# Optimization experiments

Hardware: AMD Instinct MI355X
Metric: run time of the kernel (lower is better)

## Reference

```python
import jax, jax.numpy as jnp
import numpy as np

INF = 1.0e9
B, NI, NJ = 1, 768, 768
C_NODE, C_PAIR = 512, 128
H, C_HID = 8, 32
LN_EPS = 1e-5


def _ln(x, w, b):
    m = jnp.mean(x, axis=-1, keepdims=True)
    v = jnp.mean(jnp.square(x - m), axis=-1, keepdims=True)
    return (x - m) * jax.lax.rsqrt(v + LN_EPS) * w + b


def setup_inputs() -> dict:
    key = jax.random.key(0)
    ks = jax.random.split(key, 16)
    s_node = 1.0 / np.sqrt(C_NODE)
    s_pair = 1.0 / np.sqrt(C_PAIR)
    s_hid = 1.0 / np.sqrt(H * C_HID)
    inp = {
        "node_embed_i": jax.random.normal(ks[0], (B, NI, C_NODE), jnp.float32),
        "node_embed_j": jax.random.normal(ks[1], (B, NJ, C_NODE), jnp.float32),
        "pair_embed": jax.random.normal(ks[2], (B, NI, NJ, C_PAIR), jnp.float32),
        "pair_mask": (jax.random.uniform(ks[3], (B, NI, NJ)) < 0.95).astype(jnp.float32),
        "node_mask_i": (jax.random.uniform(ks[4], (B, NI)) < 0.98).astype(jnp.float32),
        # LayerNorm params
        "ln_i_w": jnp.ones((C_NODE,), jnp.float32), "ln_i_b": jnp.zeros((C_NODE,), jnp.float32),
        "ln_j_w": jnp.ones((C_NODE,), jnp.float32), "ln_j_b": jnp.zeros((C_NODE,), jnp.float32),
        "ln_p_w": jnp.ones((C_PAIR,), jnp.float32), "ln_p_b": jnp.zeros((C_PAIR,), jnp.float32),
        # pair-bias projection and its gate: Linear(C_PAIR, H)
        "W_pb": jax.random.normal(ks[5], (C_PAIR, H), jnp.float32) * s_pair,
        "b_pb": jnp.zeros((H,), jnp.float32),
        "W_pg": jax.random.normal(ks[6], (C_PAIR, H), jnp.float32) * s_pair,
        "b_pg": jnp.zeros((H,), jnp.float32),
        # attention projections (q/k/v bias-free, OpenFold-style)
        "Wq": jax.random.normal(ks[7], (C_NODE, H * C_HID), jnp.float32) * s_node,
        "Wk": jax.random.normal(ks[8], (C_NODE, H * C_HID), jnp.float32) * s_node,
        "Wv": jax.random.normal(ks[9], (C_NODE, H * C_HID), jnp.float32) * s_node,
        # output gate and output projection
        "Wg": jax.random.normal(ks[10], (C_NODE, H * C_HID), jnp.float32) * s_node,
        "bg": jnp.zeros((H * C_HID,), jnp.float32),
        "Wo": jax.random.normal(ks[11], (H * C_HID, C_NODE), jnp.float32) * s_hid,
        "bo": jnp.zeros((C_NODE,), jnp.float32),
    }
    return inp


def reference(node_embed_i, node_embed_j, pair_embed, pair_mask, node_mask_i,
              ln_i_w, ln_i_b, ln_j_w, ln_j_b, ln_p_w, ln_p_b,
              W_pb, b_pb, W_pg, b_pg, Wq, Wk, Wv, Wg, bg, Wo, bo):
    # LayerNorms
    qx = _ln(node_embed_i, ln_i_w, ln_i_b)           # [B,NI,C_NODE]
    kx = _ln(node_embed_j, ln_j_w, ln_j_b)           # [B,NJ,C_NODE]
    p = _ln(pair_embed, ln_p_w, ln_p_b)              # [B,NI,NJ,C_PAIR]

    # additive mask bias: 0 where valid, -inf where masked; broadcast over heads
    mask_bias = (INF * (pair_mask - 1.0))[:, None, :, :]          # [B,1,NI,NJ]

    # gated pair bias -> [B,H,NI,NJ] (permute_final_dims([2,0,1]))
    pb = (p @ W_pb + b_pb) * jax.nn.sigmoid(p @ W_pg + b_pg)      # [B,NI,NJ,H]
    pair_bias = jnp.transpose(pb, (0, 3, 1, 2))

    # multi-head attention with injected biases
    q = (qx @ Wq).reshape(B, NI, H, C_HID) * (C_HID ** -0.5)
    k = (kx @ Wk).reshape(B, NJ, H, C_HID)
    v = (kx @ Wv).reshape(B, NJ, H, C_HID)
    scores = jnp.einsum('bihc,bjhc->bhij', q, k) + mask_bias + pair_bias
    a = jax.nn.softmax(scores, axis=-1)                           # [B,H,NI,NJ]
    o = jnp.einsum('bhij,bjhc->bihc', a, v)                       # [B,NI,H,C_HID]

    # sigmoid output gate, flatten heads, output projection
    g = jax.nn.sigmoid(qx @ Wg + bg).reshape(B, NI, H, C_HID)
    o = (o * g).reshape(B, NI, H * C_HID)
    mha_out = o @ Wo + bo                                         # [B,NI,C_NODE]

    # residual on the layernormed input, scaled by node mask (dropout = identity at inference)
    return qx + mha_out * node_mask_i[..., None]
```

## Files before the change

### kernel.cpp

```cpp
#include <hip/hip_runtime.h>
#include <hip/hip_bf16.h>

#define NI 768
#define NJ 768
#define CN 512
#define CP 128
#define NH 8
#define CH 32
#define HC 256

typedef float  fx4  __attribute__((ext_vector_type(4)));
typedef float  fx2  __attribute__((ext_vector_type(2)));
typedef short  bv8  __attribute__((ext_vector_type(8)));

__device__ __forceinline__ short f2bf(float f) {
    __hip_bfloat16 h = __float2bfloat16(f);
    return *reinterpret_cast<short*>(&h);
}
__device__ __forceinline__ float bf2f(unsigned short u) {
    union { unsigned int u; float f; } c; c.u = ((unsigned int)u) << 16; return c.f;
}

__global__ __launch_bounds__(256) void fused_front_kernel(
    const float* __restrict__ node_i, const float* __restrict__ node_j,
    const float* __restrict__ ln_i_w, const float* __restrict__ ln_i_b,
    const float* __restrict__ ln_j_w, const float* __restrict__ ln_j_b,
    const float* __restrict__ Wq, const float* __restrict__ Wk,
    const float* __restrict__ Wv, const float* __restrict__ Wg,
    const float* __restrict__ bg,
    const float* __restrict__ lnpw, const float* __restrict__ lnpb,
    const float* __restrict__ Wpb, const float* __restrict__ bpb,
    const float* __restrict__ Wpg, const float* __restrict__ bpg,
    const float* __restrict__ pair, const float* __restrict__ pmask,
    float* __restrict__ qx, unsigned short* __restrict__ qsb,
    unsigned short* __restrict__ ksb, unsigned short* __restrict__ vtb,
    float* __restrict__ gs, float* __restrict__ bias)
{
    const int bid = blockIdx.x;
    const int t = threadIdx.x;
    if (bid < 192) {
        __shared__ float xs[8][CN];
        __shared__ float red[4][8][2];
        const bool isj = bid >= 96;
        const int r0 = (isj ? bid - 96 : bid) * 8;
        const float* xin = isj ? node_j : node_i;
        const float* lw = isj ? ln_j_w : ln_i_w;
        const float* lb = isj ? ln_j_b : ln_i_b;
        const int wv = t >> 6;

        fx2 vrow[8]; float s8[8], q8[8];
#pragma unroll
        for (int r = 0; r < 8; ++r) {
            vrow[r] = *(const fx2*)(xin + (size_t)(r0 + r) * CN + t * 2);
            s8[r] = vrow[r][0] + vrow[r][1];
            q8[r] = vrow[r][0] * vrow[r][0] + vrow[r][1] * vrow[r][1];
        }
#pragma unroll
        for (int d = 1; d < 64; d <<= 1)
#pragma unroll
            for (int r = 0; r < 8; ++r) {
                s8[r] += __shfl_xor(s8[r], d);
                q8[r] += __shfl_xor(q8[r], d);
            }
        if ((t & 63) == 0)
#pragma unroll
            for (int r = 0; r < 8; ++r) { red[wv][r][0] = s8[r]; red[wv][r][1] = q8[r]; }
        __syncthreads();
        fx2 lwv = *(const fx2*)(lw + t * 2), lbv = *(const fx2*)(lb + t * 2);
#pragma unroll
        for (int r = 0; r < 8; ++r) {
            float s = red[0][r][0] + red[1][r][0] + red[2][r][0] + red[3][r][0];
            float q = red[0][r][1] + red[1][r][1] + red[2][r][1] + red[3][r][1];
            float mean = s * (1.f / CN);
            float var = q * (1.f / CN) - mean * mean;
            float rs = rsqrtf(var + 1e-5f);
            fx2 o;
            o[0] = (vrow[r][0] - mean) * rs * lwv[0] + lbv[0];
            o[1] = (vrow[r][1] - mean) * rs * lwv[1] + lbv[1];
            xs[r][t * 2] = o[0]; xs[r][t * 2 + 1] = o[1];
            if (!isj) *(fx2*)(qx + (size_t)(r0 + r) * CN + t * 2) = o;
        }
        __syncthreads();

        for (int m = 0; m < 2; ++m) {
            const float* W = isj ? (m ? Wv : Wk) : (m ? Wg : Wq);
            float acc[8] = {0.f,0.f,0.f,0.f,0.f,0.f,0.f,0.f};
            for (int cc = 0; cc < CN; cc += 4) {
                fx4 xv[8];
#pragma unroll
                for (int r = 0; r < 8; ++r) xv[r] = *(const fx4*)&xs[r][cc];
#pragma unroll
                for (int u = 0; u < 4; ++u) {
                    float w = W[(size_t)(cc + u) * HC + t];
#pragma unroll
                    for (int r = 0; r < 8; ++r) acc[r] = fmaf(xv[r][u], w, acc[r]);
                }
            }
            if (!isj) {
                if (m == 0) {
#pragma unroll
                    for (int r = 0; r < 8; ++r)
                        qsb[(size_t)(r0 + r) * HC + t] =
                            (unsigned short)f2bf(acc[r] * 0.17677669529663687f);
                } else {
#pragma unroll
                    for (int r = 0; r < 8; ++r)
                        gs[(size_t)(r0 + r) * HC + t] =
                            1.f / (1.f + __expf(-(acc[r] + bg[t])));
                }
            } else {
                if (m == 0) {
#pragma unroll
                    for (int r = 0; r < 8; ++r)
                        ksb[(size_t)(r0 + r) * HC + t] = (unsigned short)f2bf(acc[r]);
                } else {
                    bv8 vv;
#pragma unroll
                    for (int r = 0; r < 8; ++r) vv[r] = f2bf(acc[r]);
                    *(bv8*)&vtb[(size_t)t * NJ + r0] = vv;
                }
            }
        }
        return;
    }

    __shared__ unsigned short wcatT[16][136];
    __shared__ float redS[16][16], redC[16][16];
    __shared__ float scalS[16], scalC[16];
    {
        const int o = t & 15, cg = t >> 4;
        float pS = 0.f, pC = 0.f;
#pragma unroll
        for (int e = 0; e < 8; ++e) {
            int c = cg * 8 + e;
            float w = (o < 8) ? Wpb[c * 8 + o] : Wpg[c * 8 + (o - 8)];
            float wv = lnpw[c] * w;
            short b = f2bf(wv);
            wcatT[o][c] = (unsigned short)b;
            pS += bf2f((unsigned short)b);
            pC += lnpb[c] * w;
        }
        redS[cg][o] = pS; redC[cg][o] = pC;
        __syncthreads();
        if (t < 16) {
            float s = 0.f, c2 = 0.f;
#pragma unroll
            for (int k = 0; k < 16; ++k) { s += redS[k][t]; c2 += redC[k][t]; }
            scalS[t] = s;
            scalC[t] = c2 + ((t < 8) ? bpb[t] : bpg[t - 8]);
        }
        __syncthreads();
    }

    const int lane = t & 63;
    const int wave = t >> 6;
    const int tile = (bid - 192) * 4 + wave;
    const int i  = tile / (NJ / 16);
    const int jt = (tile % (NJ / 16)) * 16;
    const int o  = lane & 15;
    const int kq = lane >> 4;

    bv8 bfrag[4];
#pragma unroll
    for (int s = 0; s < 4; ++s)
        bfrag[s] = *(const bv8*)&wcatT[o][s * 32 + kq * 8];

    const float spb = scalS[o];
    const float cpb = scalC[o];

    const float* prow = pair + ((size_t)i * NJ + (jt + o)) * CP + kq * 8;
    fx4 x0[4], x1[4];
#pragma unroll
    for (int s = 0; s < 4; ++s) {
        x0[s] = *(const fx4*)(prow + s * 32);
        x1[s] = *(const fx4*)(prow + s * 32 + 4);
    }
    float sum = 0.f, ssq = 0.f;
    bv8 afrag[4];
#pragma unroll
    for (int s = 0; s < 4; ++s) {
#pragma unroll
        for (int u = 0; u < 4; ++u) {
            float a = x0[s][u], b = x1[s][u];
            sum += a + b;
            ssq = fmaf(a, a, ssq);
            ssq = fmaf(b, b, ssq);
            afrag[s][u]     = f2bf(a);
            afrag[s][u + 4] = f2bf(b);
        }
    }
    sum += __shfl_xor(sum, 16); ssq += __shfl_xor(ssq, 16);
    sum += __shfl_xor(sum, 32); ssq += __shfl_xor(ssq, 32);

    fx4 acc = {0.f, 0.f, 0.f, 0.f};
#pragma unroll
    for (int s = 0; s < 4; ++s)
        acc = __builtin_amdgcn_mfma_f32_16x16x32_bf16(afrag[s], bfrag[s], acc, 0, 0, 0);

#pragma unroll
    for (int r = 0; r < 4; ++r) {
        const int p = kq * 4 + r;
        float sp = __shfl(sum, p);
        float qp = __shfl(ssq, p);
        float mean = sp * (1.f / CP);
        float var  = qp * (1.f / CP) - mean * mean;
        float rstd = rsqrtf(var + 1e-5f);
        float pre  = rstd * (acc[r] - mean * spb) + cpb;
        float part = __shfl_xor(pre, 8);
        if (o < 8) {
            float sig = 1.f / (1.f + __expf(-part));
            int j = jt + p;
            float b = pre * sig + (pmask[(size_t)i * NJ + j] - 1.f) * 1.0e9f;
            bias[((size_t)o * NI + i) * NJ + j] = b;
        }
    }
}

__global__ __launch_bounds__(256) void attn_kernel(
    const short* __restrict__ qsb, const short* __restrict__ ksb,
    const short* __restrict__ vtb, const float* __restrict__ bias,
    float* __restrict__ pnum, float* __restrict__ pden)
{
    __shared__ unsigned short P[32][392];
    __shared__ float sumbuf[4][32];
    const int i0 = blockIdx.x * 32;
    const int h  = blockIdx.y;
    const int jh = blockIdx.z;
    const int jbase = jh * 384;
    const int pb = ((int)blockIdx.x * NH + h) * 2 + jh;
    const int t = threadIdx.x;
    const int w = t >> 6;
    const int lane = t & 63;
    const int rowl = lane & 15;
    const int g = lane >> 4;

    bv8 aq[2];
#pragma unroll
    for (int it = 0; it < 2; ++it)
        aq[it] = *(const bv8*)&qsb[(size_t)(i0 + it * 16 + rowl) * HC + h * CH + g * 8];

    float rs[2][4] = {{0.f,0.f,0.f,0.f},{0.f,0.f,0.f,0.f}};
    for (int jt = 0; jt < 6; ++jt) {
        const int jloc = w * 96 + jt * 16;
        const int jb = jbase + jloc;
        bv8 bk = *(const bv8*)&ksb[(size_t)(jb + rowl) * HC + h * CH + g * 8];
#pragma unroll
        for (int it = 0; it < 2; ++it) {
            fx4 acc = {0.f, 0.f, 0.f, 0.f};
            acc = __builtin_amdgcn_mfma_f32_16x16x32_bf16(aq[it], bk, acc, 0, 0, 0);
#pragma unroll
            for (int r = 0; r < 4; ++r) {
                const int il = it * 16 + g * 4 + r;
                float s = acc[r] + bias[((size_t)h * NI + (i0 + il)) * NJ + jb + rowl];
                float p = __expf(s);
                rs[it][r] += p;
                P[il][jloc + rowl] = (unsigned short)f2bf(p);
            }
        }
    }
#pragma unroll
    for (int it = 0; it < 2; ++it)
#pragma unroll
        for (int r = 0; r < 4; ++r) {
            float v = rs[it][r];
            v += __shfl_xor(v, 1); v += __shfl_xor(v, 2);
            v += __shfl_xor(v, 4); v += __shfl_xor(v, 8);
            rs[it][r] = v;
        }
    if (rowl == 0) {
#pragma unroll
        for (int it = 0; it < 2; ++it)
#pragma unroll
            for (int r = 0; r < 4; ++r)
                sumbuf[w][it * 16 + g * 4 + r] = rs[it][r];
    }
    __syncthreads();

    if (t < 32)
        pden[(size_t)pb * 32 + t] =
            sumbuf[0][t] + sumbuf[1][t] + sumbuf[2][t] + sumbuf[3][t];

    const int it = w & 1, ct = w >> 1;
    fx4 acc = {0.f, 0.f, 0.f, 0.f};
    for (int kk = 0; kk < 12; ++kk) {
        const int jloc = kk * 32;
        bv8 ap = *(const bv8*)&P[it * 16 + rowl][jloc + g * 8];
        bv8 bv = *(const bv8*)&vtb[(size_t)(h * CH + ct * 16 + rowl) * NJ + jbase + jloc + g * 8];
        acc = __builtin_amdgcn_mfma_f32_16x16x32_bf16(ap, bv, acc, 0, 0, 0);
    }
#pragma unroll
    for (int r = 0; r < 4; ++r) {
        const int il = it * 16 + g * 4 + r;
        pnum[(size_t)pb * 1024 + il * 32 + ct * 16 + rowl] = acc[r];
    }
}

__global__ __launch_bounds__(256) void combine_out_kernel(
    const float* __restrict__ pnum, const float* __restrict__ pden,
    const float* __restrict__ gs, const float* __restrict__ qx,
    const float* __restrict__ Wo, const float* __restrict__ bo,
    const float* __restrict__ mi, float* __restrict__ outp)
{
    __shared__ float ogl[2][HC];
    const int r0 = blockIdx.x * 2;
    const int t = threadIdx.x;
    const int h = t >> 5, c = t & 31;
#pragma unroll
    for (int r = 0; r < 2; ++r) {
        const int i = r0 + r;
        const int pb = ((i >> 5) * NH + h) * 2;
        const int il = i & 31;
        float n = pnum[(size_t)(pb + 0) * 1024 + il * 32 + c]
                + pnum[(size_t)(pb + 1) * 1024 + il * 32 + c];
        float d = pden[(size_t)(pb + 0) * 32 + il]
                + pden[(size_t)(pb + 1) * 32 + il];
        ogl[r][t] = n / d * gs[(size_t)i * HC + t];
    }
    __syncthreads();

    float acc[2][2] = {{0,0},{0,0}};
    for (int cc = 0; cc < HC; cc += 4) {
        fx4 xr0 = *(const fx4*)&ogl[0][cc];
        fx4 xr1 = *(const fx4*)&ogl[1][cc];
#pragma unroll
        for (int u = 0; u < 4; ++u) {
            float w0 = Wo[(size_t)(cc + u) * CN + t];
            float w1 = Wo[(size_t)(cc + u) * CN + 256 + t];
            acc[0][0] = fmaf(xr0[u], w0, acc[0][0]); acc[0][1] = fmaf(xr0[u], w1, acc[0][1]);
            acc[1][0] = fmaf(xr1[u], w0, acc[1][0]); acc[1][1] = fmaf(xr1[u], w1, acc[1][1]);
        }
    }
#pragma unroll
    for (int r = 0; r < 2; ++r) {
        float mk = mi[r0 + r];
        size_t base = (size_t)(r0 + r) * CN;
        outp[base + t]       = qx[base + t]       + (acc[r][0] + bo[t])       * mk;
        outp[base + 256 + t] = qx[base + 256 + t] + (acc[r][1] + bo[t + 256]) * mk;
    }
}

extern "C" void kernel_launch(void* const* d_in, const int* in_sizes, int n_in,
                              void* d_out, int out_size, void* d_ws, size_t ws_size,
                              hipStream_t stream)
{
    const float* node_i = (const float*)d_in[0];
    const float* node_j = (const float*)d_in[1];
    const float* pair   = (const float*)d_in[2];
    const float* pmask  = (const float*)d_in[3];
    const float* nmask  = (const float*)d_in[4];
    const float* ln_i_w = (const float*)d_in[5];
    const float* ln_i_b = (const float*)d_in[6];
    const float* ln_j_w = (const float*)d_in[7];
    const float* ln_j_b = (const float*)d_in[8];
    const float* ln_p_w = (const float*)d_in[9];
    const float* ln_p_b = (const float*)d_in[10];
    const float* W_pb   = (const float*)d_in[11];
    const float* b_pb   = (const float*)d_in[12];
    const float* W_pg   = (const float*)d_in[13];
    const float* b_pg   = (const float*)d_in[14];
    const float* Wq     = (const float*)d_in[15];
    const float* Wk     = (const float*)d_in[16];
    const float* Wv     = (const float*)d_in[17];
    const float* Wg     = (const float*)d_in[18];
    const float* bg     = (const float*)d_in[19];
    const float* Wo     = (const float*)d_in[20];
    const float* bo     = (const float*)d_in[21];
    float* outp = (float*)d_out;

    float* fw = (float*)d_ws;
    float* qx   = fw;
    float* gs   = qx + (size_t)NI * CN;
    float* bias = gs + (size_t)NI * HC;
    float* pnum = bias + (size_t)NH * NI * NJ;
    float* pden = pnum + (size_t)24 * NH * 2 * 1024;
    unsigned short* qsb = (unsigned short*)(pden + (size_t)24 * NH * 2 * 32);
    unsigned short* ksb = qsb + (size_t)NI * HC;
    unsigned short* vtb = ksb + (size_t)NJ * HC;

    hipLaunchKernelGGL(fused_front_kernel, dim3(192 + (NI * NJ) / 64), dim3(256), 0, stream,
                       node_i, node_j, ln_i_w, ln_i_b, ln_j_w, ln_j_b,
                       Wq, Wk, Wv, Wg, bg,
                       ln_p_w, ln_p_b, W_pb, b_pb, W_pg, b_pg,
                       pair, pmask,
                       qx, qsb, ksb, vtb, gs, bias);
    hipLaunchKernelGGL(attn_kernel, dim3(NI / 32, NH, 2), dim3(256), 0, stream,
                       (const short*)qsb, (const short*)ksb, (const short*)vtb,
                       bias, pnum, pden);
    hipLaunchKernelGGL(combine_out_kernel, dim3(NI / 2), dim3(256), 0, stream,
                       pnum, pden, gs, qx, Wo, bo, nmask, outp);
}
```

Baseline: 112.0 us.

## Store pair bias as bf16 via LDS-staged writes and drop split-J attention partials

The pair-bias tensor (8×768×768) is now written as bf16 instead of fp32. Each front block covers 64 contiguous j positions and stages results in shared memory so it can emit vectorized row stores instead of scattered 4-byte writes. The attention kernel no longer splits J in two. Each block handles the full 768 columns with a larger P buffer and normalizes and gates its output directly, which removes the pnum/pden partial buffers and simplifies the final projection kernel. This cuts bias write and read traffic, but it halves the attention grid and adds bf16 rounding on the bias, including the -1e9 mask values.

```diff
diff --git a/kernel.cpp b/kernel.cpp
--- a/kernel.cpp
+++ b/kernel.cpp
@@ -12,6 +12,7 @@
 typedef float  fx4  __attribute__((ext_vector_type(4)));
 typedef float  fx2  __attribute__((ext_vector_type(2)));
 typedef short  bv8  __attribute__((ext_vector_type(8)));
+typedef unsigned short usx4 __attribute__((ext_vector_type(4)));
 
 __device__ __forceinline__ short f2bf(float f) {
     __hip_bfloat16 h = __float2bfloat16(f);
@@ -34,7 +35,7 @@
     const float* __restrict__ pair, const float* __restrict__ pmask,
     float* __restrict__ qx, unsigned short* __restrict__ qsb,
     unsigned short* __restrict__ ksb, unsigned short* __restrict__ vtb,
-    float* __restrict__ gs, float* __restrict__ bias)
+    float* __restrict__ gs, unsigned short* __restrict__ biasb)
 {
     const int bid = blockIdx.x;
     const int t = threadIdx.x;
@@ -127,6 +128,7 @@
     __shared__ unsigned short wcatT[16][136];
     __shared__ float redS[16][16], redC[16][16];
     __shared__ float scalS[16], scalC[16];
+    __shared__ unsigned short sb[8][68];
     {
         const int o = t & 15, cg = t >> 4;
         float pS = 0.f, pC = 0.f;
@@ -154,9 +156,10 @@
 
     const int lane = t & 63;
     const int wave = t >> 6;
-    const int tile = (bid - 192) * 4 + wave;
-    const int i  = tile / (NJ / 16);
-    const int jt = (tile % (NJ / 16)) * 16;
+    const int bid2 = bid - 192;
+    const int i    = bid2 / 12;
+    const int jt64 = (bid2 % 12) * 64;
+    const int jt   = jt64 + wave * 16;
     const int o  = lane & 15;
     const int kq = lane >> 4;
 
@@ -211,23 +214,28 @@
             float sig = 1.f / (1.f + __expf(-part));
             int j = jt + p;
             float b = pre * sig + (pmask[(size_t)i * NJ + j] - 1.f) * 1.0e9f;
-            bias[((size_t)o * NI + i) * NJ + j] = b;
-        }
+            sb[o][wave * 16 + kq * 4 + r] = (unsigned short)f2bf(b);
+        }
+    }
+    __syncthreads();
+    if (t < 128) {
+        const int oo = t >> 4, ck = t & 15;
+        usx4 v;
+#pragma unroll
+        for (int u = 0; u < 4; ++u) v[u] = sb[oo][ck * 4 + u];
+        *(usx4*)&biasb[((size_t)oo * NI + i) * NJ + jt64 + ck * 4] = v;
     }
 }
 
 __global__ __launch_bounds__(256) void attn_kernel(
     const short* __restrict__ qsb, const short* __restrict__ ksb,
-    const short* __restrict__ vtb, const float* __restrict__ bias,
-    float* __restrict__ pnum, float* __restrict__ pden)
+    const short* __restrict__ vtb, const unsigned short* __restrict__ biasb,
+    const float* __restrict__ gs, float* __restrict__ og)
 {
-    __shared__ unsigned short P[32][392];
+    __shared__ unsigned short P[32][776];
     __shared__ float sumbuf[4][32];
     const int i0 = blockIdx.x * 32;
     const int h  = blockIdx.y;
-    const int jh = blockIdx.z;
-    const int jbase = jh * 384;
-    const int pb = ((int)blockIdx.x * NH + h) * 2 + jh;
     const int t = threadIdx.x;
     const int w = t >> 6;
     const int lane = t & 63;
@@ -239,10 +247,11 @@
     for (int it = 0; it < 2; ++it)
         aq[it] = *(const bv8*)&qsb[(size_t)(i0 + it * 16 + rowl) * HC + h * CH + g * 8];
 
+    const unsigned short* bbase = biasb + (size_t)h * NI * NJ;
     float rs[2][4] = {{0.f,0.f,0.f,0.f},{0.f,0.f,0.f,0.f}};
-    for (int jt = 0; jt < 6; ++jt) {
-        const int jloc = w * 96 + jt * 16;
-        const int jb = jbase + jloc;
+#pragma unroll 2
+    for (int jt = 0; jt < 12; ++jt) {
+        const int jb = w * 192 + jt * 16;
         bv8 bk = *(const bv8*)&ksb[(size_t)(jb + rowl) * HC + h * CH + g * 8];
 #pragma unroll
         for (int it = 0; it < 2; ++it) {
@@ -251,10 +260,10 @@
 #pragma unroll
             for (int r = 0; r < 4; ++r) {
                 const int il = it * 16 + g * 4 + r;
-                float s = acc[r] + bias[((size_t)h * NI + (i0 + il)) * NJ + jb + rowl];
+                float s = acc[r] + bf2f(bbase[(size_t)(i0 + il) * NJ + jb + rowl]);
                 float p = __expf(s);
                 rs[it][r] += p;
-                P[il][jloc + rowl] = (unsigned short)f2bf(p);
+                P[il][jb + rowl] = (unsigned short)f2bf(p);
             }
         }
     }
@@ -276,52 +285,34 @@
     }
     __syncthreads();
 
-    if (t < 32)
-        pden[(size_t)pb * 32 + t] =
-            sumbuf[0][t] + sumbuf[1][t] + sumbuf[2][t] + sumbuf[3][t];
-
     const int it = w & 1, ct = w >> 1;
     fx4 acc = {0.f, 0.f, 0.f, 0.f};
-    for (int kk = 0; kk < 12; ++kk) {
-        const int jloc = kk * 32;
-        bv8 ap = *(const bv8*)&P[it * 16 + rowl][jloc + g * 8];
-        bv8 bv = *(const bv8*)&vtb[(size_t)(h * CH + ct * 16 + rowl) * NJ + jbase + jloc + g * 8];
+    for (int kk = 0; kk < 24; ++kk) {
+        const int jb = kk * 32;
+        bv8 ap = *(const bv8*)&P[it * 16 + rowl][jb + g * 8];
+        bv8 bv = *(const bv8*)&vtb[(size_t)(h * CH + ct * 16 + rowl) * NJ + jb + g * 8];
         acc = __builtin_amdgcn_mfma_f32_16x16x32_bf16(ap, bv, acc, 0, 0, 0);
     }
 #pragma unroll
     for (int r = 0; r < 4; ++r) {
         const int il = it * 16 + g * 4 + r;
-        pnum[(size_t)pb * 1024 + il * 32 + ct * 16 + rowl] = acc[r];
-    }
-}
-
-__global__ __launch_bounds__(256) void combine_out_kernel(
-    const float* __restrict__ pnum, const float* __restrict__ pden,
-    const float* __restrict__ gs, const float* __restrict__ qx,
+        float s = sumbuf[0][il] + sumbuf[1][il] + sumbuf[2][il] + sumbuf[3][il];
+        size_t idx = (size_t)(i0 + il) * HC + h * CH + ct * 16 + rowl;
+        og[idx] = acc[r] / s * gs[idx];
+    }
+}
+
+__global__ __launch_bounds__(256) void out_proj_kernel(
+    const float* __restrict__ og, const float* __restrict__ qx,
     const float* __restrict__ Wo, const float* __restrict__ bo,
     const float* __restrict__ mi, float* __restrict__ outp)
 {
-    __shared__ float ogl[2][HC];
     const int r0 = blockIdx.x * 2;
     const int t = threadIdx.x;
-    const int h = t >> 5, c = t & 31;
-#pragma unroll
-    for (int r = 0; r < 2; ++r) {
-        const int i = r0 + r;
-        const int pb = ((i >> 5) * NH + h) * 2;
-        const int il = i & 31;
-        float n = pnum[(size_t)(pb + 0) * 1024 + il * 32 + c]
-                + pnum[(size_t)(pb + 1) * 1024 + il * 32 + c];
-        float d = pden[(size_t)(pb + 0) * 32 + il]
-                + pden[(size_t)(pb + 1) * 32 + il];
-        ogl[r][t] = n / d * gs[(size_t)i * HC + t];
-    }
-    __syncthreads();
-
     float acc[2][2] = {{0,0},{0,0}};
     for (int cc = 0; cc < HC; cc += 4) {
-        fx4 xr0 = *(const fx4*)&ogl[0][cc];
-        fx4 xr1 = *(const fx4*)&ogl[1][cc];
+        fx4 xr0 = *(const fx4*)(og + (size_t)(r0 + 0) * HC + cc);
+        fx4 xr1 = *(const fx4*)(og + (size_t)(r0 + 1) * HC + cc);
 #pragma unroll
         for (int u = 0; u < 4; ++u) {
             float w0 = Wo[(size_t)(cc + u) * CN + t];
@@ -368,24 +359,23 @@
     float* outp = (float*)d_out;
 
     float* fw = (float*)d_ws;
-    float* qx   = fw;
-    float* gs   = qx + (size_t)NI * CN;
-    float* bias = gs + (size_t)NI * HC;
-    float* pnum = bias + (size_t)NH * NI * NJ;
-    float* pden = pnum + (size_t)24 * NH * 2 * 1024;
-    unsigned short* qsb = (unsigned short*)(pden + (size_t)24 * NH * 2 * 32);
+    float* qx = fw;
+    float* gs = qx + (size_t)NI * CN;
+    float* og = gs + (size_t)NI * HC;
+    unsigned short* qsb = (unsigned short*)(og + (size_t)NI * HC);
     unsigned short* ksb = qsb + (size_t)NI * HC;
     unsigned short* vtb = ksb + (size_t)NJ * HC;
+    unsigned short* biasb = vtb + (size_t)HC * NJ;
 
     hipLaunchKernelGGL(fused_front_kernel, dim3(192 + (NI * NJ) / 64), dim3(256), 0, stream,
                        node_i, node_j, ln_i_w, ln_i_b, ln_j_w, ln_j_b,
                        Wq, Wk, Wv, Wg, bg,
                        ln_p_w, ln_p_b, W_pb, b_pb, W_pg, b_pg,
                        pair, pmask,
-                       qx, qsb, ksb, vtb, gs, bias);
-    hipLaunchKernelGGL(attn_kernel, dim3(NI / 32, NH, 2), dim3(256), 0, stream,
+                       qx, qsb, ksb, vtb, gs, biasb);
+    hipLaunchKernelGGL(attn_kernel, dim3(NI / 32, NH), dim3(256), 0, stream,
                        (const short*)qsb, (const short*)ksb, (const short*)vtb,
-                       bias, pnum, pden);
-    hipLaunchKernelGGL(combine_out_kernel, dim3(NI / 2), dim3(256), 0, stream,
-                       pnum, pden, gs, qx, Wo, bo, nmask, outp);
-}
+                       biasb, gs, og);
+    hipLaunchKernelGGL(out_proj_kernel, dim3(NI / 2), dim3(256), 0, stream,
+                       og, qx, Wo, bo, nmask, outp);
+}
```

New measurement: 115.0 us. 1.03x slower.

## Fuse pair-bias computation into attention to avoid materializing the bias tensor

Applied to the files above, without the earlier changes.

Splits node projections into their own kernel and fuses the pair layernorm/bias projection with the attention score, softmax numerator and PV product per (row, 64-column strip). This removes the write and re-read of the full fp32 [H,NI,NJ] bias tensor. In exchange the score and PV products move from bf16 MFMA to scalar fp32 FMAs with per-strip partial sums, and the final kernel has to reduce 12 strips. It also serializes the node work before the pair work instead of overlapping them in one launch.

```diff
diff --git a/kernel.cpp b/kernel.cpp
--- a/kernel.cpp
+++ b/kernel.cpp
@@ -8,6 +8,7 @@
 #define NH 8
 #define CH 32
 #define HC 256
+#define NSTRIP 12
 
 typedef float  fx4  __attribute__((ext_vector_type(4)));
 typedef float  fx2  __attribute__((ext_vector_type(2)));
@@ -21,126 +22,155 @@
     union { unsigned int u; float f; } c; c.u = ((unsigned int)u) << 16; return c.f;
 }
 
-__global__ __launch_bounds__(256) void fused_front_kernel(
+__global__ __launch_bounds__(256) void node_kernel(
     const float* __restrict__ node_i, const float* __restrict__ node_j,
     const float* __restrict__ ln_i_w, const float* __restrict__ ln_i_b,
     const float* __restrict__ ln_j_w, const float* __restrict__ ln_j_b,
     const float* __restrict__ Wq, const float* __restrict__ Wk,
     const float* __restrict__ Wv, const float* __restrict__ Wg,
     const float* __restrict__ bg,
+    float* __restrict__ qx, float* __restrict__ qs,
+    float* __restrict__ ksf, unsigned short* __restrict__ vtb,
+    float* __restrict__ gs)
+{
+    __shared__ float xs[8][CN];
+    __shared__ float red[4][8][2];
+    const int bid = blockIdx.x;
+    const int t = threadIdx.x;
+    const bool isj = bid >= 96;
+    const int r0 = (isj ? bid - 96 : bid) * 8;
+    const float* xin = isj ? node_j : node_i;
+    const float* lw = isj ? ln_j_w : ln_i_w;
+    const float* lb = isj ? ln_j_b : ln_i_b;
+    const int wv = t >> 6;
+
+    fx2 vrow[8]; float s8[8], q8[8];
+#pragma unroll
+    for (int r = 0; r < 8; ++r) {
+        vrow[r] = *(const fx2*)(xin + (size_t)(r0 + r) * CN + t * 2);
+        s8[r] = vrow[r][0] + vrow[r][1];
+        q8[r] = vrow[r][0] * vrow[r][0] + vrow[r][1] * vrow[r][1];
+    }
+#pragma unroll
+    for (int d = 1; d < 64; d <<= 1)
+#pragma unroll
+        for (int r = 0; r < 8; ++r) {
+            s8[r] += __shfl_xor(s8[r], d);
+            q8[r] += __shfl_xor(q8[r], d);
+        }
+    if ((t & 63) == 0)
+#pragma unroll
+        for (int r = 0; r < 8; ++r) { red[wv][r][0] = s8[r]; red[wv][r][1] = q8[r]; }
+    __syncthreads();
+    fx2 lwv = *(const fx2*)(lw + t * 2), lbv = *(const fx2*)(lb + t * 2);
+#pragma unroll
+    for (int r = 0; r < 8; ++r) {
+        float s = red[0][r][0] + red[1][r][0] + red[2][r][0] + red[3][r][0];
+        float q = red[0][r][1] + red[1][r][1] + red[2][r][1] + red[3][r][1];
+        float mean = s * (1.f / CN);
+        float var = q * (1.f / CN) - mean * mean;
+        float rs = rsqrtf(var + 1e-5f);
+        fx2 o;
+        o[0] = (vrow[r][0] - mean) * rs * lwv[0] + lbv[0];
+        o[1] = (vrow[r][1] - mean) * rs * lwv[1] + lbv[1];
+        xs[r][t * 2] = o[0]; xs[r][t * 2 + 1] = o[1];
+        if (!isj) *(fx2*)(qx + (size_t)(r0 + r) * CN + t * 2) = o;
+    }
+    __syncthreads();
+
+    for (int m = 0; m < 2; ++m) {
+        const float* W = isj ? (m ? Wv : Wk) : (m ? Wg : Wq);
+        float acc[8] = {0.f,0.f,0.f,0.f,0.f,0.f,0.f,0.f};
+        for (int cc = 0; cc < CN; cc += 4) {
+            fx4 xv[8];
+#pragma unroll
+            for (int r = 0; r < 8; ++r) xv[r] = *(const fx4*)&xs[r][cc];
+#pragma unroll
+            for (int u = 0; u < 4; ++u) {
+                float w = W[(size_t)(cc + u) * HC + t];
+#pragma unroll
+                for (int r = 0; r < 8; ++r) acc[r] = fmaf(xv[r][u], w, acc[r]);
+            }
+        }
+        if (!isj) {
+            if (m == 0) {
+#pragma unroll
+                for (int r = 0; r < 8; ++r)
+                    qs[(size_t)(r0 + r) * HC + t] = acc[r] * 0.17677669529663687f;
+            } else {
+#pragma unroll
+                for (int r = 0; r < 8; ++r)
+                    gs[(size_t)(r0 + r) * HC + t] =
+                        1.f / (1.f + __expf(-(acc[r] + bg[t])));
+            }
+        } else {
+            if (m == 0) {
+#pragma unroll
+                for (int r = 0; r < 8; ++r)
+                    ksf[(size_t)(r0 + r) * HC + t] = acc[r];
+            } else {
+                bv8 vv;
+#pragma unroll
+                for (int r = 0; r < 8; ++r) vv[r] = f2bf(acc[r]);
+                *(bv8*)&vtb[(size_t)t * NJ + r0] = vv;
+            }
+        }
+    }
+}
+
+__global__ __launch_bounds__(256) void flash_pair_kernel(
+    const float* __restrict__ pair, const float* __restrict__ pmask,
     const float* __restrict__ lnpw, const float* __restrict__ lnpb,
     const float* __restrict__ Wpb, const float* __restrict__ bpb,
     const float* __restrict__ Wpg, const float* __restrict__ bpg,
-    const float* __restrict__ pair, const float* __restrict__ pmask,
-    float* __restrict__ qx, unsigned short* __restrict__ qsb,
-    unsigned short* __restrict__ ksb, unsigned short* __restrict__ vtb,
-    float* __restrict__ gs, float* __restrict__ bias)
+    const float* __restrict__ qs, const float* __restrict__ ksf,
+    const unsigned short* __restrict__ vtb,
+    float* __restrict__ pnum, float* __restrict__ pden)
 {
-    const int bid = blockIdx.x;
-    const int t = threadIdx.x;
-    if (bid < 192) {
-        __shared__ float xs[8][CN];
-        __shared__ float red[4][8][2];
-        const bool isj = bid >= 96;
-        const int r0 = (isj ? bid - 96 : bid) * 8;
-        const float* xin = isj ? node_j : node_i;
-        const float* lw = isj ? ln_j_w : ln_i_w;
-        const float* lb = isj ? ln_j_b : ln_i_b;
-        const int wv = t >> 6;
-
-        fx2 vrow[8]; float s8[8], q8[8];
-#pragma unroll
-        for (int r = 0; r < 8; ++r) {
-            vrow[r] = *(const fx2*)(xin + (size_t)(r0 + r) * CN + t * 2);
-            s8[r] = vrow[r][0] + vrow[r][1];
-            q8[r] = vrow[r][0] * vrow[r][0] + vrow[r][1] * vrow[r][1];
-        }
-#pragma unroll
-        for (int d = 1; d < 64; d <<= 1)
-#pragma unroll
-            for (int r = 0; r < 8; ++r) {
-                s8[r] += __shfl_xor(s8[r], d);
-                q8[r] += __shfl_xor(q8[r], d);
-            }
-        if ((t & 63) == 0)
-#pragma unroll
-            for (int r = 0; r < 8; ++r) { red[wv][r][0] = s8[r]; red[wv][r][1] = q8[r]; }
-        __syncthreads();
-        fx2 lwv = *(const fx2*)(lw + t * 2), lbv = *(const fx2*)(lb + t * 2);
-#pragma unroll
-        for (int r = 0; r < 8; ++r) {
-            float s = red[0][r][0] + red[1][r][0] + red[2][r][0] + red[3][r][0];
-            float q = red[0][r][1] + red[1][r][1] + red[2][r][1] + red[3][r][1];
-            float mean = s * (1.f / CN);
-            float var = q * (1.f / CN) - mean * mean;
-            float rs = rsqrtf(var + 1e-5f);
-            fx2 o;
-            o[0] = (vrow[r][0] - mean) * rs * lwv[0] + lbv[0];
-            o[1] = (vrow[r][1] - mean) * rs * lwv[1] + lbv[1];
-            xs[r][t * 2] = o[0]; xs[r][t * 2 + 1] = o[1];
-            if (!isj) *(fx2*)(qx + (size_t)(r0 + r) * CN + t * 2) = o;
-        }
-        __syncthreads();
-
-        for (int m = 0; m < 2; ++m) {
-            const float* W = isj ? (m ? Wv : Wk) : (m ? Wg : Wq);
-            float acc[8] = {0.f,0.f,0.f,0.f,0.f,0.f,0.f,0.f};
-            for (int cc = 0; cc < CN; cc += 4) {
-                fx4 xv[8];
-#pragma unroll
-                for (int r = 0; r < 8; ++r) xv[r] = *(const fx4*)&xs[r][cc];
-#pragma unroll
-                for (int u = 0; u < 4; ++u) {
-                    float w = W[(size_t)(cc + u) * HC + t];
-#pragma unroll
-                    for (int r = 0; r < 8; ++r) acc[r] = fmaf(xv[r][u], w, acc[r]);
-                }
-            }
-            if (!isj) {
-                if (m == 0) {
-#pragma unroll
-                    for (int r = 0; r < 8; ++r)
-                        qsb[(size_t)(r0 + r) * HC + t] =
-                            (unsigned short)f2bf(acc[r] * 0.17677669529663687f);
-                } else {
-#pragma unroll
-                    for (int r = 0; r < 8; ++r)
-                        gs[(size_t)(r0 + r) * HC + t] =
-                            1.f / (1.f + __expf(-(acc[r] + bg[t])));
-                }
-            } else {
-                if (m == 0) {
-#pragma unroll
-                    for (int r = 0; r < 8; ++r)
-                        ksb[(size_t)(r0 + r) * HC + t] = (unsigned short)f2bf(acc[r]);
-                } else {
-                    bv8 vv;
-#pragma unroll
-                    for (int r = 0; r < 8; ++r) vv[r] = f2bf(acc[r]);
-                    *(bv8*)&vtb[(size_t)t * NJ + r0] = vv;
-                }
-            }
-        }
-        return;
-    }
-
     __shared__ unsigned short wcatT[16][136];
     __shared__ float redS[16][16], redC[16][16];
     __shared__ float scalS[16], scalC[16];
+    __shared__ float sb[8][68];
+    __shared__ float qrow[HC];
+    __shared__ float pmbuf[64];
+    __shared__ float pbuf[8][64];
+
+    const int t = threadIdx.x;
+    const int bid = blockIdx.x;
+    const int i = bid / NSTRIP;
+    const int strip = bid % NSTRIP;
+    const int jt64 = strip * 64;
+    const int lane = t & 63, wave = t >> 6;
+    const int o = lane & 15, kq = lane >> 4;
+    const int jt = jt64 + wave * 16;
+
+    const float* prow = pair + ((size_t)i * NJ + (jt + o)) * CP + kq * 8;
+    fx4 x0[4], x1[4];
+#pragma unroll
+    for (int s = 0; s < 4; ++s) {
+        x0[s] = *(const fx4*)(prow + s * 32);
+        x1[s] = *(const fx4*)(prow + s * 32 + 4);
+    }
+    const float qld = qs[(size_t)i * HC + t];
+    float pmld = 0.f;
+    if (t < 64) pmld = pmask[(size_t)i * NJ + jt64 + t];
+
     {
-        const int o = t & 15, cg = t >> 4;
+        const int oo = t & 15, cg = t >> 4;
         float pS = 0.f, pC = 0.f;
 #pragma unroll
         for (int e = 0; e < 8; ++e) {
             int c = cg * 8 + e;
-            float w = (o < 8) ? Wpb[c * 8 + o] : Wpg[c * 8 + (o - 8)];
+            float w = (oo < 8) ? Wpb[c * 8 + oo] : Wpg[c * 8 + (oo - 8)];
             float wv = lnpw[c] * w;
             short b = f2bf(wv);
-            wcatT[o][c] = (unsigned short)b;
+            wcatT[oo][c] = (unsigned short)b;
             pS += bf2f((unsigned short)b);
             pC += lnpb[c] * w;
         }
-        redS[cg][o] = pS; redC[cg][o] = pC;
+        redS[cg][oo] = pS; redC[cg][oo] = pC;
+        qrow[t] = qld;
+        if (t < 64) pmbuf[t] = pmld;
         __syncthreads();
         if (t < 16) {
             float s = 0.f, c2 = 0.f;
@@ -152,29 +182,13 @@
         __syncthreads();
     }
 
-    const int lane = t & 63;
-    const int wave = t >> 6;
-    const int tile = (bid - 192) * 4 + wave;
-    const int i  = tile / (NJ / 16);
-    const int jt = (tile % (NJ / 16)) * 16;
-    const int o  = lane & 15;
-    const int kq = lane >> 4;
-
     bv8 bfrag[4];
 #pragma unroll
     for (int s = 0; s < 4; ++s)
         bfrag[s] = *(const bv8*)&wcatT[o][s * 32 + kq * 8];
-
     const float spb = scalS[o];
     const float cpb = scalC[o];
 
-    const float* prow = pair + ((size_t)i * NJ + (jt + o)) * CP + kq * 8;
-    fx4 x0[4], x1[4];
-#pragma unroll
-    for (int s = 0; s < 4; ++s) {
-        x0[s] = *(const fx4*)(prow + s * 32);
-        x1[s] = *(const fx4*)(prow + s * 32 + 4);
-    }
     float sum = 0.f, ssq = 0.f;
     bv8 afrag[4];
 #pragma unroll
@@ -209,93 +223,56 @@
         float part = __shfl_xor(pre, 8);
         if (o < 8) {
             float sig = 1.f / (1.f + __expf(-part));
-            int j = jt + p;
-            float b = pre * sig + (pmask[(size_t)i * NJ + j] - 1.f) * 1.0e9f;
-            bias[((size_t)o * NI + i) * NJ + j] = b;
-        }
-    }
-}
-
-__global__ __launch_bounds__(256) void attn_kernel(
-    const short* __restrict__ qsb, const short* __restrict__ ksb,
-    const short* __restrict__ vtb, const float* __restrict__ bias,
-    float* __restrict__ pnum, float* __restrict__ pden)
-{
-    __shared__ unsigned short P[32][392];
-    __shared__ float sumbuf[4][32];
-    const int i0 = blockIdx.x * 32;
-    const int h  = blockIdx.y;
-    const int jh = blockIdx.z;
-    const int jbase = jh * 384;
-    const int pb = ((int)blockIdx.x * NH + h) * 2 + jh;
-    const int t = threadIdx.x;
-    const int w = t >> 6;
-    const int lane = t & 63;
-    const int rowl = lane & 15;
-    const int g = lane >> 4;
-
-    bv8 aq[2];
-#pragma unroll
-    for (int it = 0; it < 2; ++it)
-        aq[it] = *(const bv8*)&qsb[(size_t)(i0 + it * 16 + rowl) * HC + h * CH + g * 8];
-
-    float rs[2][4] = {{0.f,0.f,0.f,0.f},{0.f,0.f,0.f,0.f}};
-    for (int jt = 0; jt < 6; ++jt) {
-        const int jloc = w * 96 + jt * 16;
-        const int jb = jbase + jloc;
-        bv8 bk = *(const bv8*)&ksb[(size_t)(jb + rowl) * HC + h * CH + g * 8];
-#pragma unroll
-        for (int it = 0; it < 2; ++it) {
-            fx4 acc = {0.f, 0.f, 0.f, 0.f};
-            acc = __builtin_amdgcn_mfma_f32_16x16x32_bf16(aq[it], bk, acc, 0, 0, 0);
-#pragma unroll
-            for (int r = 0; r < 4; ++r) {
-                const int il = it * 16 + g * 4 + r;
-                float s = acc[r] + bias[((size_t)h * NI + (i0 + il)) * NJ + jb + rowl];
-                float p = __expf(s);
-                rs[it][r] += p;
-                P[il][jloc + rowl] = (unsigned short)f2bf(p);
-            }
-        }
-    }
-#pragma unroll
-    for (int it = 0; it < 2; ++it)
-#pragma unroll
-        for (int r = 0; r < 4; ++r) {
-            float v = rs[it][r];
-            v += __shfl_xor(v, 1); v += __shfl_xor(v, 2);
-            v += __shfl_xor(v, 4); v += __shfl_xor(v, 8);
-            rs[it][r] = v;
-        }
-    if (rowl == 0) {
-#pragma unroll
-        for (int it = 0; it < 2; ++it)
-#pragma unroll
-            for (int r = 0; r < 4; ++r)
-                sumbuf[w][it * 16 + g * 4 + r] = rs[it][r];
-    }
-    __syncthreads();
-
-    if (t < 32)
-        pden[(size_t)pb * 32 + t] =
-            sumbuf[0][t] + sumbuf[1][t] + sumbuf[2][t] + sumbuf[3][t];
-
-    const int it = w & 1, ct = w >> 1;
-    fx4 acc = {0.f, 0.f, 0.f, 0.f};
-    for (int kk = 0; kk < 12; ++kk) {
-        const int jloc = kk * 32;
-        bv8 ap = *(const bv8*)&P[it * 16 + rowl][jloc + g * 8];
-        bv8 bv = *(const bv8*)&vtb[(size_t)(h * CH + ct * 16 + rowl) * NJ + jbase + jloc + g * 8];
-        acc = __builtin_amdgcn_mfma_f32_16x16x32_bf16(ap, bv, acc, 0, 0, 0);
-    }
-#pragma unroll
-    for (int r = 0; r < 4; ++r) {
-        const int il = it * 16 + g * 4 + r;
-        pnum[(size_t)pb * 1024 + il * 32 + ct * 16 + rowl] = acc[r];
-    }
-}
-
-__global__ __launch_bounds__(256) void combine_out_kernel(
+            int jloc = wave * 16 + p;
+            sb[o][jloc] = pre * sig + (pmbuf[jloc] - 1.f) * 1.0e9f;
+        }
+    }
+    __syncthreads();
+
+    const int h = t >> 5, jl = t & 31;
+    fx4 qv[8];
+#pragma unroll
+    for (int u = 0; u < 8; ++u) qv[u] = *(const fx4*)&qrow[h * CH + u * 4];
+
+    const float* kp0 = ksf + (size_t)(jt64 + jl) * HC + h * CH;
+    const float* kp1 = kp0 + (size_t)32 * HC;
+    float s0 = 0.f, s1 = 0.f;
+#pragma unroll
+    for (int u = 0; u < 8; ++u) {
+        fx4 kv = *(const fx4*)(kp0 + u * 4);
+        s0 += qv[u][0]*kv[0] + qv[u][1]*kv[1] + qv[u][2]*kv[2] + qv[u][3]*kv[3];
+    }
+#pragma unroll
+    for (int u = 0; u < 8; ++u) {
+        fx4 kv = *(const fx4*)(kp1 + u * 4);
+        s1 += qv[u][0]*kv[0] + qv[u][1]*kv[1] + qv[u][2]*kv[2] + qv[u][3]*kv[3];
+    }
+    float p0 = __expf(s0 + sb[h][jl]);
+    float p1 = __expf(s1 + sb[h][jl + 32]);
+    pbuf[h][jl] = p0; pbuf[h][jl + 32] = p1;
+    float pd = p0 + p1;
+#pragma unroll
+    for (int d = 1; d < 32; d <<= 1) pd += __shfl_xor(pd, d);
+    if (jl == 0) pden[((size_t)i * NSTRIP + strip) * NH + h] = pd;
+    __syncthreads();
+
+    const int c = t & 31;
+    float ov = 0.f;
+    const unsigned short* vp = vtb + (size_t)(h * CH + c) * NJ + jt64;
+#pragma unroll
+    for (int jo = 0; jo < 8; ++jo) {
+        bv8 vv = *(const bv8*)(vp + jo * 8);
+        fx4 pa = *(const fx4*)&pbuf[h][jo * 8];
+        fx4 pb2 = *(const fx4*)&pbuf[h][jo * 8 + 4];
+        ov += pa[0]*bf2f((unsigned short)vv[0]) + pa[1]*bf2f((unsigned short)vv[1])
+            + pa[2]*bf2f((unsigned short)vv[2]) + pa[3]*bf2f((unsigned short)vv[3])
+            + pb2[0]*bf2f((unsigned short)vv[4]) + pb2[1]*bf2f((unsigned short)vv[5])
+            + pb2[2]*bf2f((unsigned short)vv[6]) + pb2[3]*bf2f((unsigned short)vv[7]);
+    }
+    pnum[((size_t)i * NSTRIP + strip) * HC + t] = ov;
+}
+
+__global__ __launch_bounds__(256) void reduce_out_kernel(
     const float* __restrict__ pnum, const float* __restrict__ pden,
     const float* __restrict__ gs, const float* __restrict__ qx,
     const float* __restrict__ Wo, const float* __restrict__ bo,
@@ -304,16 +281,16 @@
     __shared__ float ogl[2][HC];
     const int r0 = blockIdx.x * 2;
     const int t = threadIdx.x;
-    const int h = t >> 5, c = t & 31;
+    const int h = t >> 5;
 #pragma unroll
     for (int r = 0; r < 2; ++r) {
         const int i = r0 + r;
-        const int pb = ((i >> 5) * NH + h) * 2;
-        const int il = i & 31;
-        float n = pnum[(size_t)(pb + 0) * 1024 + il * 32 + c]
-                + pnum[(size_t)(pb + 1) * 1024 + il * 32 + c];
-        float d = pden[(size_t)(pb + 0) * 32 + il]
-                + pden[(size_t)(pb + 1) * 32 + il];
+        float n = 0.f, d = 0.f;
+#pragma unroll
+        for (int s = 0; s < NSTRIP; ++s) {
+            n += pnum[((size_t)i * NSTRIP + s) * HC + t];
+            d += pden[((size_t)i * NSTRIP + s) * NH + h];
+        }
         ogl[r][t] = n / d * gs[(size_t)i * HC + t];
     }
     __syncthreads();
@@ -370,22 +347,20 @@
     float* fw = (float*)d_ws;
     float* qx   = fw;
     float* gs   = qx + (size_t)NI * CN;
-    float* bias = gs + (size_t)NI * HC;
-    float* pnum = bias + (size_t)NH * NI * NJ;
-    float* pden = pnum + (size_t)24 * NH * 2 * 1024;
-    unsigned short* qsb = (unsigned short*)(pden + (size_t)24 * NH * 2 * 32);
-    unsigned short* ksb = qsb + (size_t)NI * HC;
-    unsigned short* vtb = ksb + (size_t)NJ * HC;
-
-    hipLaunchKernelGGL(fused_front_kernel, dim3(192 + (NI * NJ) / 64), dim3(256), 0, stream,
+    float* qs   = gs + (size_t)NI * HC;
+    float* ksf  = qs + (size_t)NI * HC;
+    float* pnum = ksf + (size_t)NJ * HC;
+    float* pden = pnum + (size_t)NI * NSTRIP * HC;
+    unsigned short* vtb = (unsigned short*)(pden + (size_t)NI * NSTRIP * NH);
+
+    hipLaunchKernelGGL(node_kernel, dim3(192), dim3(256), 0, stream,
                        node_i, node_j, ln_i_w, ln_i_b, ln_j_w, ln_j_b,
                        Wq, Wk, Wv, Wg, bg,
+                       qx, qs, ksf, vtb, gs);
+    hipLaunchKernelGGL(flash_pair_kernel, dim3(NI * NSTRIP), dim3(256), 0, stream,
+                       pair, pmask,
                        ln_p_w, ln_p_b, W_pb, b_pb, W_pg, b_pg,
-                       pair, pmask,
-                       qx, qsb, ksb, vtb, gs, bias);
-    hipLaunchKernelGGL(attn_kernel, dim3(NI / 32, NH, 2), dim3(256), 0, stream,
-                       (const short*)qsb, (const short*)ksb, (const short*)vtb,
-                       bias, pnum, pden);
-    hipLaunchKernelGGL(combine_out_kernel, dim3(NI / 2), dim3(256), 0, stream,
+                       qs, ksf, vtb, pnum, pden);
+    hipLaunchKernelGGL(reduce_out_kernel, dim3(NI / 2), dim3(256), 0, stream,
                        pnum, pden, gs, qx, Wo, bo, nmask, outp);
 }
```

New measurement: 219.9 us. 96.3% more time.

## Store pair bias as bf16 with LDS-staged coalesced writes and MFMA LayerNorm stats

Applied to the files above, without the earlier changes.

The pair-bias tensor is now written and read as bf16 rather than fp32, halving the 18 MB intermediate traffic between the front and attention kernels. Bias writes are staged through shared memory so each block emits contiguous 64-element rows per head, instead of scattered 4-byte stores. Pair-row loads are hoisted above the weight-preparation prologue to overlap global latency. The LayerNorm sum and sum of squares are computed with extra MFMAs on the bf16 fragments (ones vector and a self product), which trades fp32 statistics for bf16-rounded ones and adds precision risk to the -1e9 mask and variance terms.

```diff
diff --git a/kernel.cpp b/kernel.cpp
--- a/kernel.cpp
+++ b/kernel.cpp
@@ -12,6 +12,7 @@
 typedef float  fx4  __attribute__((ext_vector_type(4)));
 typedef float  fx2  __attribute__((ext_vector_type(2)));
 typedef short  bv8  __attribute__((ext_vector_type(8)));
+typedef unsigned short usx4 __attribute__((ext_vector_type(4)));
 
 __device__ __forceinline__ short f2bf(float f) {
     __hip_bfloat16 h = __float2bfloat16(f);
@@ -34,7 +35,7 @@
     const float* __restrict__ pair, const float* __restrict__ pmask,
     float* __restrict__ qx, unsigned short* __restrict__ qsb,
     unsigned short* __restrict__ ksb, unsigned short* __restrict__ vtb,
-    float* __restrict__ gs, float* __restrict__ bias)
+    float* __restrict__ gs, unsigned short* __restrict__ biasb)
 {
     const int bid = blockIdx.x;
     const int t = threadIdx.x;
@@ -127,20 +128,39 @@
     __shared__ unsigned short wcatT[16][136];
     __shared__ float redS[16][16], redC[16][16];
     __shared__ float scalS[16], scalC[16];
+    __shared__ unsigned short sb[8][68];
+
+    const int lane = t & 63;
+    const int wave = t >> 6;
+    const int bid2 = bid - 192;
+    const int i    = bid2 / 12;
+    const int jt64 = (bid2 % 12) * 64;
+    const int jt   = jt64 + wave * 16;
+    const int o  = lane & 15;
+    const int kq = lane >> 4;
+
+    const float* prow = pair + ((size_t)i * NJ + (jt + o)) * CP + kq * 8;
+    fx4 x0[4], x1[4];
+#pragma unroll
+    for (int s = 0; s < 4; ++s) {
+        x0[s] = *(const fx4*)(prow + s * 32);
+        x1[s] = *(const fx4*)(prow + s * 32 + 4);
+    }
+
     {
-        const int o = t & 15, cg = t >> 4;
+        const int oo = t & 15, cg = t >> 4;
         float pS = 0.f, pC = 0.f;
 #pragma unroll
         for (int e = 0; e < 8; ++e) {
             int c = cg * 8 + e;
-            float w = (o < 8) ? Wpb[c * 8 + o] : Wpg[c * 8 + (o - 8)];
+            float w = (oo < 8) ? Wpb[c * 8 + oo] : Wpg[c * 8 + (oo - 8)];
             float wv = lnpw[c] * w;
             short b = f2bf(wv);
-            wcatT[o][c] = (unsigned short)b;
+            wcatT[oo][c] = (unsigned short)b;
             pS += bf2f((unsigned short)b);
             pC += lnpb[c] * w;
         }
-        redS[cg][o] = pS; redC[cg][o] = pC;
+        redS[cg][oo] = pS; redC[cg][oo] = pC;
         __syncthreads();
         if (t < 16) {
             float s = 0.f, c2 = 0.f;
@@ -152,56 +172,41 @@
         __syncthreads();
     }
 
-    const int lane = t & 63;
-    const int wave = t >> 6;
-    const int tile = (bid - 192) * 4 + wave;
-    const int i  = tile / (NJ / 16);
-    const int jt = (tile % (NJ / 16)) * 16;
-    const int o  = lane & 15;
-    const int kq = lane >> 4;
-
     bv8 bfrag[4];
 #pragma unroll
     for (int s = 0; s < 4; ++s)
         bfrag[s] = *(const bv8*)&wcatT[o][s * 32 + kq * 8];
-
     const float spb = scalS[o];
     const float cpb = scalC[o];
 
-    const float* prow = pair + ((size_t)i * NJ + (jt + o)) * CP + kq * 8;
-    fx4 x0[4], x1[4];
+    bv8 afrag[4];
 #pragma unroll
     for (int s = 0; s < 4; ++s) {
-        x0[s] = *(const fx4*)(prow + s * 32);
-        x1[s] = *(const fx4*)(prow + s * 32 + 4);
-    }
-    float sum = 0.f, ssq = 0.f;
-    bv8 afrag[4];
+#pragma unroll
+        for (int u = 0; u < 4; ++u) {
+            afrag[s][u]     = f2bf(x0[s][u]);
+            afrag[s][u + 4] = f2bf(x1[s][u]);
+        }
+    }
+    bv8 ones;
+#pragma unroll
+    for (int u = 0; u < 8; ++u) ones[u] = (short)0x3F80;
+
+    fx4 acc  = {0.f, 0.f, 0.f, 0.f};
+    fx4 accS = {0.f, 0.f, 0.f, 0.f};
+    fx4 accG = {0.f, 0.f, 0.f, 0.f};
 #pragma unroll
     for (int s = 0; s < 4; ++s) {
-#pragma unroll
-        for (int u = 0; u < 4; ++u) {
-            float a = x0[s][u], b = x1[s][u];
-            sum += a + b;
-            ssq = fmaf(a, a, ssq);
-            ssq = fmaf(b, b, ssq);
-            afrag[s][u]     = f2bf(a);
-            afrag[s][u + 4] = f2bf(b);
-        }
-    }
-    sum += __shfl_xor(sum, 16); ssq += __shfl_xor(ssq, 16);
-    sum += __shfl_xor(sum, 32); ssq += __shfl_xor(ssq, 32);
-
-    fx4 acc = {0.f, 0.f, 0.f, 0.f};
-#pragma unroll
-    for (int s = 0; s < 4; ++s)
-        acc = __builtin_amdgcn_mfma_f32_16x16x32_bf16(afrag[s], bfrag[s], acc, 0, 0, 0);
+        acc  = __builtin_amdgcn_mfma_f32_16x16x32_bf16(afrag[s], bfrag[s], acc,  0, 0, 0);
+        accS = __builtin_amdgcn_mfma_f32_16x16x32_bf16(afrag[s], ones,     accS, 0, 0, 0);
+        accG = __builtin_amdgcn_mfma_f32_16x16x32_bf16(afrag[s], afrag[s], accG, 0, 0, 0);
+    }
 
 #pragma unroll
     for (int r = 0; r < 4; ++r) {
         const int p = kq * 4 + r;
-        float sp = __shfl(sum, p);
-        float qp = __shfl(ssq, p);
+        float sp = accS[r];
+        float qp = __shfl(accG[r], kq * 20 + r);
         float mean = sp * (1.f / CP);
         float var  = qp * (1.f / CP) - mean * mean;
         float rstd = rsqrtf(var + 1e-5f);
@@ -211,14 +216,22 @@
             float sig = 1.f / (1.f + __expf(-part));
             int j = jt + p;
             float b = pre * sig + (pmask[(size_t)i * NJ + j] - 1.f) * 1.0e9f;
-            bias[((size_t)o * NI + i) * NJ + j] = b;
-        }
+            sb[o][wave * 16 + p] = (unsigned short)f2bf(b);
+        }
+    }
+    __syncthreads();
+    if (t < 128) {
+        const int oo = t >> 4, ck = t & 15;
+        usx4 v;
+#pragma unroll
+        for (int u = 0; u < 4; ++u) v[u] = sb[oo][ck * 4 + u];
+        *(usx4*)&biasb[((size_t)oo * NI + i) * NJ + jt64 + ck * 4] = v;
     }
 }
 
 __global__ __launch_bounds__(256) void attn_kernel(
     const short* __restrict__ qsb, const short* __restrict__ ksb,
-    const short* __restrict__ vtb, const float* __restrict__ bias,
+    const short* __restrict__ vtb, const unsigned short* __restrict__ biasb,
     float* __restrict__ pnum, float* __restrict__ pden)
 {
     __shared__ unsigned short P[32][392];
@@ -239,6 +252,7 @@
     for (int it = 0; it < 2; ++it)
         aq[it] = *(const bv8*)&qsb[(size_t)(i0 + it * 16 + rowl) * HC + h * CH + g * 8];
 
+    const unsigned short* bbase = biasb + (size_t)h * NI * NJ;
     float rs[2][4] = {{0.f,0.f,0.f,0.f},{0.f,0.f,0.f,0.f}};
     for (int jt = 0; jt < 6; ++jt) {
         const int jloc = w * 96 + jt * 16;
@@ -251,7 +265,7 @@
 #pragma unroll
             for (int r = 0; r < 4; ++r) {
                 const int il = it * 16 + g * 4 + r;
-                float s = acc[r] + bias[((size_t)h * NI + (i0 + il)) * NJ + jb + rowl];
+                float s = acc[r] + bf2f(bbase[(size_t)(i0 + il) * NJ + jb + rowl]);
                 float p = __expf(s);
                 rs[it][r] += p;
                 P[il][jloc + rowl] = (unsigned short)f2bf(p);
@@ -370,22 +384,22 @@
     float* fw = (float*)d_ws;
     float* qx   = fw;
     float* gs   = qx + (size_t)NI * CN;
-    float* bias = gs + (size_t)NI * HC;
-    float* pnum = bias + (size_t)NH * NI * NJ;
+    float* pnum = gs + (size_t)NI * HC;
     float* pden = pnum + (size_t)24 * NH * 2 * 1024;
     unsigned short* qsb = (unsigned short*)(pden + (size_t)24 * NH * 2 * 32);
     unsigned short* ksb = qsb + (size_t)NI * HC;
     unsigned short* vtb = ksb + (size_t)NJ * HC;
+    unsigned short* biasb = vtb + (size_t)HC * NJ;
 
     hipLaunchKernelGGL(fused_front_kernel, dim3(192 + (NI * NJ) / 64), dim3(256), 0, stream,
                        node_i, node_j, ln_i_w, ln_i_b, ln_j_w, ln_j_b,
                        Wq, Wk, Wv, Wg, bg,
                        ln_p_w, ln_p_b, W_pb, b_pb, W_pg, b_pg,
                        pair, pmask,
-                       qx, qsb, ksb, vtb, gs, bias);
+                       qx, qsb, ksb, vtb, gs, biasb);
     hipLaunchKernelGGL(attn_kernel, dim3(NI / 32, NH, 2), dim3(256), 0, stream,
                        (const short*)qsb, (const short*)ksb, (const short*)vtb,
-                       bias, pnum, pden);
+                       biasb, pnum, pden);
     hipLaunchKernelGGL(combine_out_kernel, dim3(NI / 2), dim3(256), 0, stream,
                        pnum, pden, gs, qx, Wo, bo, nmask, outp);
 }
```

Result: faster. 108.9 us (-2.8%).
